# Performance work log

Measured on AMD Instinct MI355X. Metric: run time of the kernel, lower is better.

The kernel has to match this reference:

```python
import jax, jax.numpy as jnp
import numpy as np

EPS_CLAMP = 1e-6
TAU2 = 1.0


def _l2norm_rows(x):
    # F.normalize(x, p=2, dim=1) with eps=1e-12
    n = jnp.sqrt(jnp.sum(x * x, axis=1, keepdims=True))
    return x / jnp.maximum(n, 1e-12)


def _ws_v22(x_mean, x_std):
    m = _l2norm_rows(x_mean)                      # [N, F]
    c = _l2norm_rows(jnp.exp(x_std))              # [N, F]
    sq = jnp.sum(m * m, axis=1)                   # [N]
    # squared euclidean pairwise distance (cdist(...)**2)
    d2 = jnp.maximum(sq[:, None] + sq[None, :] - 2.0 * (m @ m.T), 0.0)
    csum = jnp.sum(c, axis=1)                     # [N]
    cs = jnp.sqrt(c)
    res = d2 + csum[:, None] + csum[None, :] - 2.0 * (cs @ cs.T)
    return jnp.exp(-res)                          # [N, N]


def _gcn_conv_dense(A, x, W, b):
    # PyG GCNConv with dense weighted adjacency A (A[i,j] = weight of edge i->j),
    # add_remaining_self_loops(fill=1), deg over target (column sums),
    # norm_ij = d_i^-1/2 * A_ij * d_j^-1/2, aggregate at target: out = A_norm^T @ (xW) + b
    diag = jnp.diagonal(A)
    A = A + jnp.diag(jnp.where(diag > 0, 0.0, 1.0))  # add self-loop weight 1 only where missing
    deg = jnp.sum(A, axis=0)                         # column sums (target degree)
    dis = jnp.where(deg > 0, deg ** -0.5, 0.0)
    An = dis[:, None] * A * dis[None, :]
    return An.T @ (x @ W) + b


def _encoder(A, x, W0, b0, W1, b1):
    h = jax.nn.relu(_gcn_conv_dense(A, x, W0, b0))
    return jax.nn.relu(_gcn_conv_dense(A, h, W1, b1))


def setup_inputs() -> dict:
    key = jax.random.key(0)
    ks = jax.random.split(key, 16)
    N, F, H = 4096, 512, 256
    s_in = 1.0 / np.sqrt(F)
    s_h = 1.0 / np.sqrt(2 * H)
    inp = {
        "x": jax.random.normal(ks[0], (N, F), dtype=jnp.float32),
        "new_edge": jax.random.uniform(ks[1], (N, N), dtype=jnp.float32),
        "beta": jax.random.uniform(ks[2], (1,), dtype=jnp.float32),
        "delta": jax.random.uniform(ks[3], (1,), dtype=jnp.float32),
        "eps": jax.random.uniform(ks[4], (N, N), dtype=jnp.float32),
        "Wm": jax.random.uniform(ks[5], (F, F), jnp.float32, -s_in, s_in),
        "bm": jax.random.uniform(ks[6], (F,), jnp.float32, -s_in, s_in),
        "Ws": jax.random.uniform(ks[7], (F, F), jnp.float32, -s_in, s_in),
        "bs": jax.random.uniform(ks[8], (F,), jnp.float32, -s_in, s_in),
        "mW0": jax.random.uniform(ks[9], (F, 2 * H), jnp.float32, -s_in, s_in) ,
        "mb0": jnp.zeros((2 * H,), jnp.float32),
        "mW1": jax.random.uniform(ks[10], (2 * H, H), jnp.float32, -s_h, s_h),
        "mb1": jnp.zeros((H,), jnp.float32),
        "sW0": jax.random.uniform(ks[11], (F, 2 * H), jnp.float32, -s_in, s_in),
        "sb0": jnp.zeros((2 * H,), jnp.float32),
        "sW1": jax.random.uniform(ks[12], (2 * H, H), jnp.float32, -s_h, s_h),
        "sb1": jnp.zeros((H,), jnp.float32),
    }
    return inp


def reference(x, new_edge, beta, delta, eps, Wm, bm, Ws, bs,
              mW0, mb0, mW1, mb1, sW0, sb0, sW1, sb1):
    b = beta[0]
    d = delta[0]
    x_mean = x @ Wm + bm
    x_std = x @ Ws + bs
    ws = _l2norm_rows(_ws_v22(x_mean, x_std))       # F.normalize(WS_v22(...)) row-wise
    term = (1.0 - b) * ws + b * new_edge
    term = jnp.clip(term, EPS_CLAMP, 1.0 - EPS_CLAMP)
    term = jnp.log(term / (1.0 - term))
    e = jnp.clip(eps, EPS_CLAMP, 1.0 - EPS_CLAMP)
    term = term + jnp.log(e / (1.0 - e))
    term = jax.nn.sigmoid(term / TAU2)
    term = jnp.where(term > d, term, 0.0)           # dense sparsified adjacency
    z_mean = _encoder(term, x_mean, mW0, mb0, mW1, mb1)
    z_std = _encoder(term, x_std, sW0, sb0, sW1, sb1)
    return z_mean, z_std
```

## Files before the change

### kernel.cpp

```cpp
#include <hip/hip_runtime.h>
#include <cstddef>

static constexpr int kN = 4096;
static constexpr int kF = 512;
static constexpr int kH = 256;
static constexpr float kClamp = 1e-6f;

using bf16x8 = __attribute__((ext_vector_type(8))) __bf16;
using f32x4 = __attribute__((ext_vector_type(4))) float;
using ushort8 = __attribute__((ext_vector_type(8))) unsigned short;
using ushort4v = __attribute__((ext_vector_type(4))) unsigned short;

static constexpr size_t PLANE_XF = (size_t)kN * kF;
static constexpr size_t PLANE_NN = (size_t)kN * kN;
static constexpr size_t PLANE_W = (size_t)512 * 512;
static constexpr size_t PLANE_W1 = (size_t)256 * 512;
static constexpr size_t PLANE_V0 = (size_t)1024 * kN;
static constexpr size_t PLANE_H = (size_t)kN * 1024;
static constexpr size_t PLANE_V1 = (size_t)512 * kN;

__device__ __forceinline__ unsigned short f2bf(float x) {
  unsigned int u = __float_as_uint(x);
  u += 0x7fffu + ((u >> 16) & 1u);
  return (unsigned short)(u >> 16);
}
__device__ __forceinline__ float bf2f(unsigned short h) {
  return __uint_as_float(((unsigned int)h) << 16);
}
__device__ __forceinline__ void split3(float x, unsigned short& h,
                                       unsigned short& m, unsigned short& l) {
  h = f2bf(x);
  const float r1 = x - bf2f(h);
  m = f2bf(r1);
  l = f2bf(r1 - bf2f(m));
}
__device__ __forceinline__ void split2(float x, unsigned short& h,
                                       unsigned short& m) {
  h = f2bf(x);
  m = f2bf(x - bf2f(h));
}
__device__ __forceinline__ void split2x4(const float4 v, ushort4v& h4,
                                         ushort4v& m4) {
  unsigned short h, m;
  split2(v.x, h, m); h4.x = h; m4.x = m;
  split2(v.y, h, m); h4.y = h; m4.y = m;
  split2(v.z, h, m); h4.z = h; m4.z = m;
  split2(v.w, h, m); h4.w = h; m4.w = m;
}

__device__ __forceinline__ bf16x8 ldfrag(const unsigned short* p) {
  ushort8 r = *(const ushort8*)p;
  return __builtin_bit_cast(bf16x8, r);
}
__device__ __forceinline__ f32x4 mfma16(bf16x8 a, bf16x8 b, f32x4 c) {
  return __builtin_amdgcn_mfma_f32_16x16x32_bf16(a, b, c, 0, 0, 0);
}
__device__ __forceinline__ f32x4 mfma_split6(const bf16x8* a3, const bf16x8* b3,
                                             f32x4 acc) {
  acc = mfma16(a3[2], b3[0], acc);
  acc = mfma16(a3[0], b3[2], acc);
  acc = mfma16(a3[1], b3[1], acc);
  acc = mfma16(a3[1], b3[0], acc);
  acc = mfma16(a3[0], b3[1], acc);
  acc = mfma16(a3[0], b3[0], acc);
  return acc;
}

__device__ __forceinline__ void tri_map(int b, int& bi, int& bj) {
  int x = (int)((sqrtf(8.0f * (float)b + 1.0f) - 1.0f) * 0.5f);
  while ((x + 1) * (x + 2) / 2 <= b) ++x;
  while (x * (x + 1) / 2 > b) --x;
  bi = x;
  bj = b - x * (x + 1) / 2;
}

__device__ __forceinline__ float block_reduce_sum(float v, float* sbuf) {
  const int tid = threadIdx.x;
  sbuf[tid] = v;
  __syncthreads();
#pragma unroll
  for (int s = 128; s > 0; s >>= 1) {
    if (tid < s) sbuf[tid] += sbuf[tid + s];
    __syncthreads();
  }
  const float r = sbuf[0];
  __syncthreads();
  return r;
}

__global__ __launch_bounds__(256) void prep_w(
    const float* s0, const float* s1, const float* s2, const float* s3,
    const float* s4, const float* s5, unsigned short* d0, unsigned short* d1,
    unsigned short* d2, unsigned short* d3, unsigned short* d4,
    unsigned short* d5) {
  const int seg = blockIdx.y;
  const float* src;
  unsigned short* dst;
  int N;
  bool tri;
  switch (seg) {
    case 0: src = s0; dst = d0; N = 512; tri = true; break;
    case 1: src = s1; dst = d1; N = 512; tri = true; break;
    case 2: src = s2; dst = d2; N = 512; tri = false; break;
    case 3: src = s3; dst = d3; N = 512; tri = false; break;
    case 4: src = s4; dst = d4; N = 256; tri = false; break;
    default: src = s5; dst = d5; N = 256; tri = false; break;
  }
  const int id = blockIdx.x * 256 + threadIdx.x;
  if (id >= 512 * N) return;
  const int k = id & 511;
  const int n = id >> 9;
  const float v = src[(size_t)k * N + n];
  const size_t base = (size_t)n * 512 + k;
  const size_t plane = (size_t)512 * N;
  if (tri) {
    unsigned short h, m, l;
    split3(v, h, m, l);
    dst[base] = h;
    dst[plane + base] = m;
    dst[2 * plane + base] = l;
  } else {
    unsigned short h, m;
    split2(v, h, m);
    dst[base] = h;
    dst[plane + base] = m;
  }
}

__global__ __launch_bounds__(256) void split_x(const float* __restrict__ x,
                                               unsigned short* __restrict__ x3) {
  const size_t id = (size_t)blockIdx.x * 256 + threadIdx.x;
  unsigned short h, m, l;
  split3(x[id], h, m, l);
  x3[id] = h;
  x3[PLANE_XF + id] = m;
  x3[2 * PLANE_XF + id] = l;
}

__global__ __launch_bounds__(256) void gemm_x(
    const unsigned short* __restrict__ A3, const unsigned short* __restrict__ B30,
    const unsigned short* __restrict__ B31, float* __restrict__ C0,
    float* __restrict__ C1, const float* __restrict__ bias0,
    const float* __restrict__ bias1) {
  constexpr int BM = 128, BN = 64, K = 512;
  __shared__ __align__(16) unsigned short Asl[3][BM][40];
  __shared__ __align__(16) unsigned short Bsl[3][BN][40];
  const int tid = threadIdx.x;
  const int lane = tid & 63;
  const int wave = tid >> 6;
  const int wm = wave >> 1, wn = wave & 1;
  const int m0 = blockIdx.y * BM;
  const int n0 = blockIdx.x * BN;
  const bool str1 = (n0 >= 512);
  const int nloc = str1 ? (n0 - 512) : n0;
  const unsigned short* Bb = str1 ? B31 : B30;
  const float* bias = str1 ? bias1 : bias0;
  float* C = str1 ? C1 : C0;
  const int rl = lane & 15;
  const int kq = (lane >> 4) * 8;
  const int q = lane >> 4;

  f32x4 acc[4][2];
#pragma unroll
  for (int i = 0; i < 4; ++i)
#pragma unroll
    for (int j = 0; j < 2; ++j) acc[i][j] = (f32x4){0.f, 0.f, 0.f, 0.f};

  for (int k0 = 0; k0 < K; k0 += 32) {
#pragma unroll
    for (int it = 0; it < 6; ++it) {
      const int c = tid + it * 256;
      const int plane = c / (BM * 4);
      const int rem = c % (BM * 4);
      const int row = rem >> 2;
      const int kc = (rem & 3) * 8;
      const ushort8 v = *(const ushort8*)(&A3[(size_t)plane * PLANE_XF +
                                              (size_t)(m0 + row) * K + k0 + kc]);
      *(ushort8*)(&Asl[plane][row][kc]) = v;
    }
#pragma unroll
    for (int it = 0; it < 3; ++it) {
      const int c = tid + it * 256;
      const int plane = c / (BN * 4);
      const int rem = c % (BN * 4);
      const int row = rem >> 2;
      const int kc = (rem & 3) * 8;
      const ushort8 v = *(const ushort8*)(&Bb[(size_t)plane * PLANE_W +
                                              (size_t)(nloc + row) * K + k0 + kc]);
      *(ushort8*)(&Bsl[plane][row][kc]) = v;
    }
    __syncthreads();
    bf16x8 af[4][3], bfr[2][3];
#pragma unroll
    for (int mt = 0; mt < 4; ++mt)
#pragma unroll
      for (int t = 0; t < 3; ++t)
        af[mt][t] = ldfrag(&Asl[t][wm * 64 + mt * 16 + rl][kq]);
#pragma unroll
    for (int nt = 0; nt < 2; ++nt)
#pragma unroll
      for (int t = 0; t < 3; ++t)
        bfr[nt][t] = ldfrag(&Bsl[t][wn * 32 + nt * 16 + rl][kq]);
#pragma unroll
    for (int mt = 0; mt < 4; ++mt)
#pragma unroll
      for (int nt = 0; nt < 2; ++nt)
        acc[mt][nt] = mfma_split6(af[mt], bfr[nt], acc[mt][nt]);
    __syncthreads();
  }
#pragma unroll
  for (int mt = 0; mt < 4; ++mt)
#pragma unroll
    for (int nt = 0; nt < 2; ++nt) {
      const int col = nloc + wn * 32 + nt * 16 + rl;
      const int row0 = m0 + wm * 64 + mt * 16 + q * 4;
      const float bv = bias[col];
#pragma unroll
      for (int r = 0; r < 4; ++r)
        C[(size_t)(row0 + r) * 512 + col] = acc[mt][nt][r] + bv;
    }
}

template <int BM, int BN>
__global__ __launch_bounds__(256) void gemm2ct(
    const unsigned short* __restrict__ A0, const unsigned short* __restrict__ A1,
    int lda, size_t planeA, const unsigned short* __restrict__ B0,
    const unsigned short* __restrict__ B1, int ldb, size_t planeB,
    unsigned short* __restrict__ Cs0, unsigned short* __restrict__ Cs1, int ldc,
    size_t planeC, int N1, int K, const float* __restrict__ rowScale) {
  __shared__ __align__(16) unsigned short Asl[2][BM][40];
  __shared__ __align__(16) unsigned short Bsl[2][BN][40];
  const int tid = threadIdx.x;
  const int lane = tid & 63;
  const int wave = tid >> 6;
  const int wm = wave >> 1, wn = wave & 1;
  const int m0 = blockIdx.y * BM;
  const int n0 = blockIdx.x * BN;
  const bool str1 = (n0 >= N1);
  const int nloc = str1 ? (n0 - N1) : n0;
  const unsigned short* Ab = str1 ? A1 : A0;
  const unsigned short* Bb = str1 ? B1 : B0;
  const int rl = lane & 15;
  const int kq = (lane >> 4) * 8;
  const int q = lane >> 4;
  constexpr int MT = BM / 32;
  constexpr int NT = BN / 32;

  f32x4 acc[MT][NT];
#pragma unroll
  for (int i = 0; i < MT; ++i)
#pragma unroll
    for (int j = 0; j < NT; ++j) acc[i][j] = (f32x4){0.f, 0.f, 0.f, 0.f};

  for (int k0 = 0; k0 < K; k0 += 32) {
    constexpr int AIT = (2 * BM * 4) / 256;
#pragma unroll
    for (int it = 0; it < AIT; ++it) {
      const int c = tid + it * 256;
      const int plane = c / (BM * 4);
      const int rem = c % (BM * 4);
      const int row = rem >> 2;
      const int kc = (rem & 3) * 8;
      const ushort8 v = *(const ushort8*)(&Ab[(size_t)plane * planeA +
                                              (size_t)(m0 + row) * lda + k0 + kc]);
      *(ushort8*)(&Asl[plane][row][kc]) = v;
    }
    constexpr int BIT = (2 * BN * 4) / 256;
#pragma unroll
    for (int it = 0; it < BIT; ++it) {
      const int c = tid + it * 256;
      const int plane = c / (BN * 4);
      const int rem = c % (BN * 4);
      const int row = rem >> 2;
      const int kc = (rem & 3) * 8;
      const ushort8 v = *(const ushort8*)(&Bb[(size_t)plane * planeB +
                                              (size_t)(nloc + row) * ldb + k0 + kc]);
      *(ushort8*)(&Bsl[plane][row][kc]) = v;
    }
    __syncthreads();
    bf16x8 af[MT][2];
#pragma unroll
    for (int mt = 0; mt < MT; ++mt)
#pragma unroll
      for (int t = 0; t < 2; ++t)
        af[mt][t] = ldfrag(&Asl[t][wm * (BM / 2) + mt * 16 + rl][kq]);
#pragma unroll
    for (int nt = 0; nt < NT; ++nt) {
      const bf16x8 b0 = ldfrag(&Bsl[0][wn * (BN / 2) + nt * 16 + rl][kq]);
      const bf16x8 b1 = ldfrag(&Bsl[1][wn * (BN / 2) + nt * 16 + rl][kq]);
#pragma unroll
      for (int mt = 0; mt < MT; ++mt) {
        acc[mt][nt] = mfma16(af[mt][1], b0, acc[mt][nt]);
        acc[mt][nt] = mfma16(af[mt][0], b1, acc[mt][nt]);
        acc[mt][nt] = mfma16(af[mt][0], b0, acc[mt][nt]);
      }
    }
    __syncthreads();
  }

#pragma unroll
  for (int mt = 0; mt < MT; ++mt) {
#pragma unroll
    for (int nt = 0; nt < NT; ++nt) {
      const int colL = nloc + wn * (BN / 2) + nt * 16 + rl;
      const int row0 = m0 + wm * (BM / 2) + mt * 16 + q * 4;
      float4 v4;
      float* vp = &v4.x;
#pragma unroll
      for (int r = 0; r < 4; ++r) {
        float v = acc[mt][nt][r];
        if (rowScale) v *= rowScale[row0 + r];
        vp[r] = v;
      }
      unsigned short* C = str1 ? Cs1 : Cs0;
      ushort4v h4, m4;
      split2x4(v4, h4, m4);
      const size_t base = (size_t)colL * ldc + row0;
      *(ushort4v*)(&C[base]) = h4;
      *(ushort4v*)(&C[planeC + base]) = m4;
    }
  }
}

template <int BM, int BN, int GX, int GYP, int GZ>
__global__ __launch_bounds__(256) void gemm2k(
    const unsigned short* __restrict__ A, int lda, size_t planeA,
    const unsigned short* __restrict__ B, int ldb, size_t planeB,
    float* __restrict__ Cp, int ldc, int Mtot, int Ksl) {
  __shared__ __align__(16) unsigned short Asl[2][BM][40];
  __shared__ __align__(16) unsigned short Bsl[2][BN][40];
  const int lin = blockIdx.x;
  const int xcd = lin & 7;
  const int s = lin >> 3;
  constexpr int per = GX * GYP;
  const int z = s / per;
  const int r = s - z * per;
  const int bx = r % GX;
  const int by = xcd * GYP + r / GX;
  const int m0 = by * BM;
  const int n0 = bx * BN;
  const int kOff = z * Ksl;

  const int tid = threadIdx.x;
  const int lane = tid & 63;
  const int wave = tid >> 6;
  const int wm = wave >> 1, wn = wave & 1;
  const int rl = lane & 15;
  const int kq = (lane >> 4) * 8;
  const int q = lane >> 4;
  constexpr int MT = BM / 32;
  constexpr int NT = BN / 32;

  f32x4 acc[MT][NT];
#pragma unroll
  for (int i = 0; i < MT; ++i)
#pragma unroll
    for (int j = 0; j < NT; ++j) acc[i][j] = (f32x4){0.f, 0.f, 0.f, 0.f};

  for (int k0 = 0; k0 < Ksl; k0 += 32) {
    constexpr int AIT = (2 * BM * 4) / 256;
#pragma unroll
    for (int it = 0; it < AIT; ++it) {
      const int c = tid + it * 256;
      const int plane = c / (BM * 4);
      const int rem = c % (BM * 4);
      const int row = rem >> 2;
      const int kc = (rem & 3) * 8;
      const ushort8 v = *(const ushort8*)(&A[(size_t)plane * planeA +
                                             (size_t)(m0 + row) * lda + kOff +
                                             k0 + kc]);
      *(ushort8*)(&Asl[plane][row][kc]) = v;
    }
    constexpr int BIT = (2 * BN * 4) / 256;
#pragma unroll
    for (int it = 0; it < BIT; ++it) {
      const int c = tid + it * 256;
      const int plane = c / (BN * 4);
      const int rem = c % (BN * 4);
      const int row = rem >> 2;
      const int kc = (rem & 3) * 8;
      const ushort8 v = *(const ushort8*)(&B[(size_t)plane * planeB +
                                             (size_t)(n0 + row) * ldb + kOff +
                                             k0 + kc]);
      *(ushort8*)(&Bsl[plane][row][kc]) = v;
    }
    __syncthreads();
    bf16x8 af[MT][2];
#pragma unroll
    for (int mt = 0; mt < MT; ++mt)
#pragma unroll
      for (int t = 0; t < 2; ++t)
        af[mt][t] = ldfrag(&Asl[t][wm * (BM / 2) + mt * 16 + rl][kq]);
#pragma unroll
    for (int nt = 0; nt < NT; ++nt) {
      const bf16x8 b0 = ldfrag(&Bsl[0][wn * (BN / 2) + nt * 16 + rl][kq]);
      const bf16x8 b1 = ldfrag(&Bsl[1][wn * (BN / 2) + nt * 16 + rl][kq]);
#pragma unroll
      for (int mt = 0; mt < MT; ++mt) {
        acc[mt][nt] = mfma16(af[mt][1], b0, acc[mt][nt]);
        acc[mt][nt] = mfma16(af[mt][0], b1, acc[mt][nt]);
        acc[mt][nt] = mfma16(af[mt][0], b0, acc[mt][nt]);
      }
    }
    __syncthreads();
  }

  const size_t zoff = (size_t)z * (size_t)Mtot * (size_t)ldc;
#pragma unroll
  for (int mt = 0; mt < MT; ++mt) {
#pragma unroll
    for (int nt = 0; nt < NT; ++nt) {
      const int colL = n0 + wn * (BN / 2) + nt * 16 + rl;
      const int row0 = m0 + wm * (BM / 2) + mt * 16 + q * 4;
#pragma unroll
      for (int r = 0; r < 4; ++r)
        Cp[zoff + (size_t)(row0 + r) * ldc + colL] = acc[mt][nt][r];
    }
  }
}

__global__ __launch_bounds__(256) void row_stats(
    const float* __restrict__ XMf, const float* __restrict__ XSf,
    unsigned short* __restrict__ M2, unsigned short* __restrict__ CS2,
    unsigned short* __restrict__ XM2, unsigned short* __restrict__ XS2,
    float* __restrict__ sq, float* __restrict__ csum) {
  __shared__ float sbuf[256];
  const int i = blockIdx.x;
  const int tid = threadIdx.x;
  const size_t base = (size_t)i * kF;
  const size_t i0 = base + tid, i1 = base + tid + 256;
  const float x0 = XMf[i0], x1 = XMf[i1];
  {
    unsigned short h, m;
    split2(x0, h, m);
    XM2[i0] = h; XM2[PLANE_XF + i0] = m;
    split2(x1, h, m);
    XM2[i1] = h; XM2[PLANE_XF + i1] = m;
  }
  const float nrm = block_reduce_sum(x0 * x0 + x1 * x1, sbuf);
  const float inv = 1.0f / fmaxf(sqrtf(nrm), 1e-12f);
  const float m0 = x0 * inv, m1 = x1 * inv;
  {
    unsigned short h, m;
    split2(m0, h, m);
    M2[i0] = h; M2[PLANE_XF + i0] = m;
    split2(m1, h, m);
    M2[i1] = h; M2[PLANE_XF + i1] = m;
  }
  const float s2 = block_reduce_sum(m0 * m0 + m1 * m1, sbuf);
  if (tid == 0) sq[i] = s2;

  const float y0 = XSf[i0], y1 = XSf[i1];
  {
    unsigned short h, m;
    split2(y0, h, m);
    XS2[i0] = h; XS2[PLANE_XF + i0] = m;
    split2(y1, h, m);
    XS2[i1] = h; XS2[PLANE_XF + i1] = m;
  }
  const float e0 = expf(y0), e1 = expf(y1);
  const float nrm2 = block_reduce_sum(e0 * e0 + e1 * e1, sbuf);
  const float inv2 = 1.0f / fmaxf(sqrtf(nrm2), 1e-12f);
  const float c0 = e0 * inv2, c1 = e1 * inv2;
  const float sc = block_reduce_sum(c0 + c1, sbuf);
  if (tid == 0) csum[i] = sc;
  {
    unsigned short h, m;
    split2(sqrtf(c0), h, m);
    CS2[i0] = h; CS2[PLANE_XF + i0] = m;
    split2(sqrtf(c1), h, m);
    CS2[i1] = h; CS2[PLANE_XF + i1] = m;
  }
}

__global__ __launch_bounds__(256) void ws_mfma2(
    const unsigned short* __restrict__ M2, const unsigned short* __restrict__ CS2,
    const float* __restrict__ sq, const float* __restrict__ csum,
    float* __restrict__ WSR) {
  __shared__ __align__(16) unsigned short S[4][2][64][40];
  int bi, bj;
  tri_map(blockIdx.x, bi, bj);
  const int i0 = bi * 64, j0 = bj * 64;
  const int tid = threadIdx.x;
  const int lane = tid & 63;
  const int wave = tid >> 6;
  const int wm = wave >> 1, wn = wave & 1;
  const int rl = lane & 15;
  const int kq = (lane >> 4) * 8;
  const int q = lane >> 4;

  f32x4 aM[2][2], aC[2][2];
#pragma unroll
  for (int i = 0; i < 2; ++i)
#pragma unroll
    for (int j = 0; j < 2; ++j) {
      aM[i][j] = (f32x4){0.f, 0.f, 0.f, 0.f};
      aC[i][j] = (f32x4){0.f, 0.f, 0.f, 0.f};
    }

  for (int k0 = 0; k0 < kF; k0 += 32) {
#pragma unroll
    for (int it = 0; it < 8; ++it) {
      const int c = tid + it * 256;
      const int op = c >> 9;
      const int rem = c & 511;
      const int plane = rem >> 8;
      const int r2 = rem & 255;
      const int row = r2 >> 2;
      const int kc = (r2 & 3) * 8;
      const unsigned short* mat = (op & 1) ? CS2 : M2;
      const int rowoff = (op < 2) ? i0 : j0;
      const ushort8 v = *(const ushort8*)(&mat[(size_t)plane * PLANE_XF +
                                               (size_t)(rowoff + row) * kF + k0 +
                                               kc]);
      *(ushort8*)(&S[op][plane][row][kc]) = v;
    }
    __syncthreads();
    bf16x8 am[2][2], ac[2][2], bm[2][2], bc[2][2];
#pragma unroll
    for (int mt = 0; mt < 2; ++mt)
#pragma unroll
      for (int t = 0; t < 2; ++t) {
        am[mt][t] = ldfrag(&S[0][t][wm * 32 + mt * 16 + rl][kq]);
        ac[mt][t] = ldfrag(&S[1][t][wm * 32 + mt * 16 + rl][kq]);
      }
#pragma unroll
    for (int nt = 0; nt < 2; ++nt)
#pragma unroll
      for (int t = 0; t < 2; ++t) {
        bm[nt][t] = ldfrag(&S[2][t][wn * 32 + nt * 16 + rl][kq]);
        bc[nt][t] = ldfrag(&S[3][t][wn * 32 + nt * 16 + rl][kq]);
      }
#pragma unroll
    for (int mt = 0; mt < 2; ++mt)
#pragma unroll
      for (int nt = 0; nt < 2; ++nt) {
        aM[mt][nt] = mfma16(am[mt][1], bm[nt][0], aM[mt][nt]);
        aM[mt][nt] = mfma16(am[mt][0], bm[nt][1], aM[mt][nt]);
        aM[mt][nt] = mfma16(am[mt][0], bm[nt][0], aM[mt][nt]);
        aC[mt][nt] = mfma16(ac[mt][1], bc[nt][0], aC[mt][nt]);
        aC[mt][nt] = mfma16(ac[mt][0], bc[nt][1], aC[mt][nt]);
        aC[mt][nt] = mfma16(ac[mt][0], bc[nt][0], aC[mt][nt]);
      }
    __syncthreads();
  }

#pragma unroll
  for (int mt = 0; mt < 2; ++mt) {
#pragma unroll
    for (int nt = 0; nt < 2; ++nt) {
      const int j = j0 + wn * 32 + nt * 16 + rl;
      const int ib = i0 + wm * 32 + mt * 16 + q * 4;
      const float sqj = sq[j], csj = csum[j];
      float4 vv;
      float* vp = &vv.x;
#pragma unroll
      for (int r = 0; r < 4; ++r) {
        const int i = ib + r;
        const float d2 = fmaxf(sq[i] + sqj - 2.0f * aM[mt][nt][r], 0.0f);
        const float res = d2 + csum[i] + csj - 2.0f * aC[mt][nt][r];
        const float v = expf(-res);
        vp[r] = v;
        WSR[(size_t)i * kN + j] = v;
      }
      if (bi != bj) *(float4*)(&WSR[(size_t)j * kN + ib]) = vv;
    }
  }
}

__global__ __launch_bounds__(256) void row_invnorm_kernel(
    const float* __restrict__ WSR, float* __restrict__ invn) {
  __shared__ float sbuf[256];
  const int i = blockIdx.x;
  const int tid = threadIdx.x;
  const float4* rp = (const float4*)(WSR + (size_t)i * kN);
  float s = 0.0f;
#pragma unroll
  for (int q = 0; q < (kN / 4) / 256; ++q) {
    const float4 v = rp[tid + q * 256];
    s += v.x * v.x + v.y * v.y + v.z * v.z + v.w * v.w;
  }
  s = block_reduce_sum(s, sbuf);
  if (tid == 0) invn[i] = 1.0f / fmaxf(sqrtf(s), 1e-12f);
}

__device__ __forceinline__ float adj_val(float w, float inv, float nev, float ev,
                                         float b, float d, bool diag) {
  float t = (1.0f - b) * (w * inv) + b * nev;
  t = fminf(fmaxf(t, kClamp), 1.0f - kClamp);
  float L = logf(t / (1.0f - t));
  const float e = fminf(fmaxf(ev, kClamp), 1.0f - kClamp);
  L += logf(e / (1.0f - e));
  const float s = 1.0f / (1.0f + expf(-L));
  float v = (s > d) ? s : 0.0f;
  if (diag) v = (v > 0.0f) ? v : 1.0f;
  return v;
}

__global__ __launch_bounds__(256) void adj_transpose(
    const float* __restrict__ WSR, const float* __restrict__ invn,
    const float* __restrict__ ne, const float* __restrict__ epsm,
    const float* __restrict__ beta_p, const float* __restrict__ delta_p,
    unsigned short* __restrict__ Adj2, float* __restrict__ degp) {
  __shared__ float T0[64][65];
  __shared__ float T1[64][65];
  const float b = beta_p[0];
  const float d = delta_p[0];
  int bi, bj;
  tri_map(blockIdx.x, bi, bj);
  const int i0 = bi * 64, j0 = bj * 64;
  const int tid = threadIdx.x;
  const int rlq = tid >> 4;
  const int cq = (tid & 15) * 4;
#pragma unroll
  for (int p = 0; p < 4; ++p) {
    const int ii = p * 16 + rlq;
    {
      const size_t off = (size_t)(i0 + ii) * kN + j0 + cq;
      const float4 w4 = *(const float4*)(&WSR[off]);
      const float4 n4 = *(const float4*)(&ne[off]);
      const float4 e4 = *(const float4*)(&epsm[off]);
      const float inv = invn[i0 + ii];
      const float wv[4] = {w4.x, w4.y, w4.z, w4.w};
      const float nv[4] = {n4.x, n4.y, n4.z, n4.w};
      const float ev[4] = {e4.x, e4.y, e4.z, e4.w};
#pragma unroll
      for (int u = 0; u < 4; ++u)
        T0[ii][cq + u] =
            adj_val(wv[u], inv, nv[u], ev[u], b, d, (i0 + ii) == (j0 + cq + u));
    }
    if (bi != bj) {
      const size_t off = (size_t)(j0 + ii) * kN + i0 + cq;
      const float4 w4 = *(const float4*)(&WSR[off]);
      const float4 n4 = *(const float4*)(&ne[off]);
      const float4 e4 = *(const float4*)(&epsm[off]);
      const float inv = invn[j0 + ii];
      const float wv[4] = {w4.x, w4.y, w4.z, w4.w};
      const float nv[4] = {n4.x, n4.y, n4.z, n4.w};
      const float ev[4] = {e4.x, e4.y, e4.z, e4.w};
#pragma unroll
      for (int u = 0; u < 4; ++u)
        T1[ii][cq + u] = adj_val(wv[u], inv, nv[u], ev[u], b, d, false);
    }
  }
  __syncthreads();
#pragma unroll
  for (int p = 0; p < 4; ++p) {
    const int jj = p * 16 + rlq;
    {
      const float4 v4 = make_float4(T0[cq + 0][jj], T0[cq + 1][jj],
                                    T0[cq + 2][jj], T0[cq + 3][jj]);
      ushort4v h4, m4;
      split2x4(v4, h4, m4);
      const size_t base = (size_t)(j0 + jj) * kN + i0 + cq;
      *(ushort4v*)(&Adj2[base]) = h4;
      *(ushort4v*)(&Adj2[PLANE_NN + base]) = m4;
    }
    if (bi != bj) {
      const float4 v4 = make_float4(T1[cq + 0][jj], T1[cq + 1][jj],
                                    T1[cq + 2][jj], T1[cq + 3][jj]);
      ushort4v h4, m4;
      split2x4(v4, h4, m4);
      const size_t base = (size_t)(i0 + jj) * kN + j0 + cq;
      *(ushort4v*)(&Adj2[base]) = h4;
      *(ushort4v*)(&Adj2[PLANE_NN + base]) = m4;
    }
  }
  if (tid < 64) {
    float s = 0.0f;
#pragma unroll 8
    for (int ii = 0; ii < 64; ++ii) s += T0[ii][tid];
    degp[(size_t)bi * kN + j0 + tid] = s;
    if (bi != bj) {
      float s1 = 0.0f;
#pragma unroll 8
      for (int ii = 0; ii < 64; ++ii) s1 += T1[ii][tid];
      degp[(size_t)bj * kN + i0 + tid] = s1;
    }
  }
}

__global__ __launch_bounds__(256) void deg_dis_kernel(
    const float* __restrict__ degp, float* __restrict__ dis) {
  const int j = blockIdx.x * 256 + threadIdx.x;
  float s = 0.0f;
#pragma unroll
  for (int c = 0; c < 64; ++c) s += degp[(size_t)c * kN + j];
  dis[j] = (s > 0.0f) ? (1.0f / sqrtf(s)) : 0.0f;
}

__global__ __launch_bounds__(256) void combine_h(
    const float* __restrict__ hp, const float* __restrict__ dis,
    const float* __restrict__ b0, const float* __restrict__ b1,
    unsigned short* __restrict__ h2) {
  const size_t qd = (size_t)blockIdx.x * 256 + threadIdx.x;
  const int m = (int)(qd >> 8);
  const int c0 = (int)(qd & 255) * 4;
  const size_t off = (size_t)m * 1024 + c0;
  const float4 s0 = *(const float4*)(&hp[off]);
  const float4 s1 = *(const float4*)(&hp[PLANE_H + off]);
  const float4 s2 = *(const float4*)(&hp[2 * PLANE_H + off]);
  const float4 s3 = *(const float4*)(&hp[3 * PLANE_H + off]);
  const float4 bv = (c0 < 512) ? *(const float4*)(&b0[c0])
                               : *(const float4*)(&b1[c0 - 512]);
  const float ds = dis[m];
  float4 v4;
  v4.x = fmaxf(ds * (s0.x + s1.x + s2.x + s3.x) + bv.x, 0.f);
  v4.y = fmaxf(ds * (s0.y + s1.y + s2.y + s3.y) + bv.y, 0.f);
  v4.z = fmaxf(ds * (s0.z + s1.z + s2.z + s3.z) + bv.z, 0.f);
  v4.w = fmaxf(ds * (s0.w + s1.w + s2.w + s3.w) + bv.w, 0.f);
  ushort4v h4, m4;
  split2x4(v4, h4, m4);
  *(ushort4v*)(&h2[off]) = h4;
  *(ushort4v*)(&h2[PLANE_H + off]) = m4;
}

__global__ __launch_bounds__(256) void combine_z(
    const float* __restrict__ zp, const float* __restrict__ dis,
    const float* __restrict__ b0, const float* __restrict__ b1,
    float* __restrict__ out) {
  const size_t qd = (size_t)blockIdx.x * 256 + threadIdx.x;
  const int m = (int)(qd >> 7);
  const int c0 = (int)(qd & 127) * 4;
  const size_t off = (size_t)m * 512 + c0;
  constexpr size_t PZ = (size_t)kN * 512;
  const float4 s0 = *(const float4*)(&zp[off]);
  const float4 s1 = *(const float4*)(&zp[PZ + off]);
  const float4 s2 = *(const float4*)(&zp[2 * PZ + off]);
  const float4 s3 = *(const float4*)(&zp[3 * PZ + off]);
  const float4 bv = (c0 < 256) ? *(const float4*)(&b0[c0])
                               : *(const float4*)(&b1[c0 - 256]);
  const float ds = dis[m];
  float4 v4;
  v4.x = fmaxf(ds * (s0.x + s1.x + s2.x + s3.x) + bv.x, 0.f);
  v4.y = fmaxf(ds * (s0.y + s1.y + s2.y + s3.y) + bv.y, 0.f);
  v4.z = fmaxf(ds * (s0.z + s1.z + s2.z + s3.z) + bv.z, 0.f);
  v4.w = fmaxf(ds * (s0.w + s1.w + s2.w + s3.w) + bv.w, 0.f);
  float* dst = (c0 < 256) ? &out[(size_t)m * 256 + c0]
                          : &out[(size_t)kN * 256 + (size_t)m * 256 + (c0 - 256)];
  *(float4*)dst = v4;
}

extern "C" void kernel_launch(void* const* d_in, const int* in_sizes, int n_in,
                              void* d_out, int out_size, void* d_ws,
                              size_t ws_size, hipStream_t stream) {
  const float* x = (const float*)d_in[0];
  const float* ne = (const float*)d_in[1];
  const float* beta = (const float*)d_in[2];
  const float* delta = (const float*)d_in[3];
  const float* epsm = (const float*)d_in[4];
  const float* Wm = (const float*)d_in[5];
  const float* bm = (const float*)d_in[6];
  const float* Ws = (const float*)d_in[7];
  const float* bs = (const float*)d_in[8];
  const float* mW0 = (const float*)d_in[9];
  const float* mb0 = (const float*)d_in[10];
  const float* mW1 = (const float*)d_in[11];
  const float* mb1 = (const float*)d_in[12];
  const float* sW0 = (const float*)d_in[13];
  const float* sb0 = (const float*)d_in[14];
  const float* sW1 = (const float*)d_in[15];
  const float* sb1 = (const float*)d_in[16];
  float* out = (float*)d_out;

  char* p = (char*)d_ws;
  float* WSR = (float*)p;                     p += PLANE_NN * 4;
  unsigned short* Adj2 = (unsigned short*)p;  p += 2 * PLANE_NN * 2;
  unsigned short* x3 = (unsigned short*)p;    p += 3 * PLANE_XF * 2;
  float* XMf = (float*)p;                     p += PLANE_XF * 4;
  float* XSf = (float*)p;                     p += PLANE_XF * 4;
  unsigned short* XM2 = (unsigned short*)p;   p += 2 * PLANE_XF * 2;
  unsigned short* XS2 = (unsigned short*)p;   p += 2 * PLANE_XF * 2;
  unsigned short* M2 = (unsigned short*)p;    p += 2 * PLANE_XF * 2;
  unsigned short* CS2 = (unsigned short*)p;   p += 2 * PLANE_XF * 2;
  unsigned short* Wm3 = (unsigned short*)p;   p += 3 * PLANE_W * 2;
  unsigned short* Ws3 = (unsigned short*)p;   p += 3 * PLANE_W * 2;
  unsigned short* mW0t2 = (unsigned short*)p; p += 2 * PLANE_W * 2;
  unsigned short* sW0t2 = (unsigned short*)p; p += 2 * PLANE_W * 2;
  unsigned short* mW1t2 = (unsigned short*)p; p += 2 * PLANE_W1 * 2;
  unsigned short* sW1t2 = (unsigned short*)p; p += 2 * PLANE_W1 * 2;
  float* degp = (float*)p;                    p += (size_t)64 * kN * 4;
  float* sq = (float*)p;                      p += kN * 4;
  float* csum = (float*)p;                    p += kN * 4;
  float* invn = (float*)p;                    p += kN * 4;
  float* dis = (float*)p;                     p += kN * 4;

  float* hp = WSR;
  float* zp = WSR;
  unsigned short* V1t2 = x3;
  unsigned short* h2 = XM2;
  unsigned short* V0t2 = M2;

  const dim3 blk(256);
  const int nTri = (kN / 64) * (kN / 64 + 1) / 2;

  prep_w<<<dim3(1024, 6), blk, 0, stream>>>(Wm, Ws, mW0, sW0, mW1, sW1, Wm3,
                                            Ws3, mW0t2, sW0t2, mW1t2, sW1t2);
  split_x<<<(kN * kF) / 256, blk, 0, stream>>>(x, x3);

  gemm_x<<<dim3(16, 32), blk, 0, stream>>>(x3, Wm3, Ws3, XMf, XSf, bm, bs);

  row_stats<<<kN, blk, 0, stream>>>(XMf, XSf, M2, CS2, XM2, XS2, sq, csum);

  ws_mfma2<<<nTri, blk, 0, stream>>>(M2, CS2, sq, csum, WSR);

  row_invnorm_kernel<<<kN, blk, 0, stream>>>(WSR, invn);

  adj_transpose<<<nTri, blk, 0, stream>>>(WSR, invn, ne, epsm, beta, delta,
                                          Adj2, degp);
  deg_dis_kernel<<<kN / 256, blk, 0, stream>>>(degp, dis);

  gemm2ct<128, 64><<<dim3(16, 32), blk, 0, stream>>>(
      XM2, XS2, kF, PLANE_XF, mW0t2, sW0t2, kF, PLANE_W, V0t2,
      V0t2 + (size_t)512 * kN, kN, PLANE_V0, 512, kF, dis);

  gemm2k<128, 128, 8, 4, 4><<<1024, blk, 0, stream>>>(
      Adj2, kN, PLANE_NN, V0t2, kN, PLANE_V0, hp, 1024, kN, kN / 4);
  combine_h<<<(int)(PLANE_H / 4 / 256), blk, 0, stream>>>(hp, dis, mb0, sb0, h2);

  gemm2ct<64, 64><<<dim3(8, 64), blk, 0, stream>>>(
      h2, h2 + 512, 1024, PLANE_H, mW1t2, sW1t2, kF, PLANE_W1, V1t2,
      V1t2 + (size_t)256 * kN, kN, PLANE_V1, 256, kF, dis);

  gemm2k<128, 128, 4, 4, 4><<<512, blk, 0, stream>>>(
      Adj2, kN, PLANE_NN, V1t2, kN, PLANE_V1, zp, 512, kN, kN / 4);
  combine_z<<<(int)((size_t)kN * 512 / 4 / 256), blk, 0, stream>>>(zp, dis, mb1,
                                                                   sb1, out);
}
```

Measured before the change: 634.1 us.

## Rewrite adjacency GEMM as 256x256 tiled, 8-wave, double-buffered direct-to-LDS pipeline

Replaces the 128x128 split-K adjacency GEMM with a 512-thread kernel that computes 256x256 tiles. It stages A and B straight into LDS with global_load_lds and double-buffers them, interleaving the refills with four MFMA phases per k-step that use setprio and barriers. The second GEMM raises split-K from 4 to 8 so the grid stays at 256 blocks, and combine_z now sums 8 partial planes. This aims to raise data reuse per tile and overlap memory with MFMA, at the cost of more partial-sum traffic in the second stage, tight vmcnt bookkeeping and heavy register pressure.

```diff
diff --git a/kernel.cpp b/kernel.cpp
--- a/kernel.cpp
+++ b/kernel.cpp
@@ -64,6 +64,13 @@
   acc = mfma16(a3[0], b3[1], acc);
   acc = mfma16(a3[0], b3[0], acc);
   return acc;
+}
+
+__device__ __forceinline__ void gload16(const unsigned short* g,
+                                        unsigned short* l) {
+  __builtin_amdgcn_global_load_lds(
+      (const __attribute__((address_space(1))) void*)g,
+      (__attribute__((address_space(3))) void*)l, 16, 0, 0);
 }
 
 __device__ __forceinline__ void tri_map(int b, int& bi, int& bj) {
@@ -322,13 +329,32 @@
   }
 }
 
-template <int BM, int BN, int GX, int GYP, int GZ>
-__global__ __launch_bounds__(256) void gemm2k(
+#define GK8_READ_A(P, AF)                                                   \
+  {                                                                         \
+    _Pragma("unroll") for (int e = 0; e < 2; ++e)                           \
+        _Pragma("unroll") for (int pl = 0; pl < 2; ++pl)                    \
+            AF[e][pl] = ldfrag(&Abuf[cur][P][pl][wm][e * 16 + rl][kq]);     \
+  }
+#define GK8_MFMA(P, AF)                                                     \
+  {                                                                         \
+    _Pragma("unroll") for (int e = 0; e < 2; ++e)                           \
+        _Pragma("unroll") for (int nt = 0; nt < 4; ++nt) {                  \
+      acc[2 * (P) + e][nt] =                                                \
+          mfma16(AF[e][1], bfr[nt][0], acc[2 * (P) + e][nt]);               \
+      acc[2 * (P) + e][nt] =                                                \
+          mfma16(AF[e][0], bfr[nt][1], acc[2 * (P) + e][nt]);               \
+      acc[2 * (P) + e][nt] =                                                \
+          mfma16(AF[e][0], bfr[nt][0], acc[2 * (P) + e][nt]);               \
+    }                                                                       \
+  }
+
+template <int GX, int GYP, int GZ>
+__global__ __launch_bounds__(512, 2) void gemm2k8(
     const unsigned short* __restrict__ A, int lda, size_t planeA,
     const unsigned short* __restrict__ B, int ldb, size_t planeB,
     float* __restrict__ Cp, int ldc, int Mtot, int Ksl) {
-  __shared__ __align__(16) unsigned short Asl[2][BM][40];
-  __shared__ __align__(16) unsigned short Bsl[2][BN][40];
+  __shared__ __align__(16) unsigned short Abuf[2][4][2][2][32][32];
+  __shared__ __align__(16) unsigned short Bbuf[2][2][256][32];
   const int lin = blockIdx.x;
   const int xcd = lin & 7;
   const int s = lin >> 3;
@@ -337,84 +363,123 @@
   const int r = s - z * per;
   const int bx = r % GX;
   const int by = xcd * GYP + r / GX;
-  const int m0 = by * BM;
-  const int n0 = bx * BN;
+  const int m0 = by * 256;
+  const int n0 = bx * 256;
   const int kOff = z * Ksl;
+  const int ntk = Ksl >> 5;
 
   const int tid = threadIdx.x;
   const int lane = tid & 63;
   const int wave = tid >> 6;
-  const int wm = wave >> 1, wn = wave & 1;
+  const int wm = wave >> 2;
+  const int wn = wave & 3;
   const int rl = lane & 15;
   const int kq = (lane >> 4) * 8;
   const int q = lane >> 4;
-  constexpr int MT = BM / 32;
-  constexpr int NT = BN / 32;
-
-  f32x4 acc[MT][NT];
-#pragma unroll
-  for (int i = 0; i < MT; ++i)
-#pragma unroll
-    for (int j = 0; j < NT; ++j) acc[i][j] = (f32x4){0.f, 0.f, 0.f, 0.f};
-
-  for (int k0 = 0; k0 < Ksl; k0 += 32) {
-    constexpr int AIT = (2 * BM * 4) / 256;
-#pragma unroll
-    for (int it = 0; it < AIT; ++it) {
-      const int c = tid + it * 256;
-      const int plane = c / (BM * 4);
-      const int rem = c % (BM * 4);
-      const int row = rem >> 2;
-      const int kc = (rem & 3) * 8;
-      const ushort8 v = *(const ushort8*)(&A[(size_t)plane * planeA +
-                                             (size_t)(m0 + row) * lda + kOff +
-                                             k0 + kc]);
-      *(ushort8*)(&Asl[plane][row][kc]) = v;
-    }
-    constexpr int BIT = (2 * BN * 4) / 256;
-#pragma unroll
-    for (int it = 0; it < BIT; ++it) {
-      const int c = tid + it * 256;
-      const int plane = c / (BN * 4);
-      const int rem = c % (BN * 4);
-      const int row = rem >> 2;
-      const int kc = (rem & 3) * 8;
-      const ushort8 v = *(const ushort8*)(&B[(size_t)plane * planeB +
-                                             (size_t)(n0 + row) * ldb + kOff +
-                                             k0 + kc]);
-      *(ushort8*)(&Bsl[plane][row][kc]) = v;
-    }
-    __syncthreads();
-    bf16x8 af[MT][2];
-#pragma unroll
-    for (int mt = 0; mt < MT; ++mt)
-#pragma unroll
-      for (int t = 0; t < 2; ++t)
-        af[mt][t] = ldfrag(&Asl[t][wm * (BM / 2) + mt * 16 + rl][kq]);
-#pragma unroll
-    for (int nt = 0; nt < NT; ++nt) {
-      const bf16x8 b0 = ldfrag(&Bsl[0][wn * (BN / 2) + nt * 16 + rl][kq]);
-      const bf16x8 b1 = ldfrag(&Bsl[1][wn * (BN / 2) + nt * 16 + rl][kq]);
-#pragma unroll
-      for (int mt = 0; mt < MT; ++mt) {
-        acc[mt][nt] = mfma16(af[mt][1], b0, acc[mt][nt]);
-        acc[mt][nt] = mfma16(af[mt][0], b1, acc[mt][nt]);
-        acc[mt][nt] = mfma16(af[mt][0], b0, acc[mt][nt]);
-      }
-    }
-    __syncthreads();
+
+  const int stRow = tid >> 2;
+  const int stSlot = (tid & 3) * 8;
+  const int aPl = tid >> 8;
+  const int aHalf = (tid >> 7) & 1;
+  const int aR = (tid >> 2) & 31;
+
+  auto stageB = [&](int bi, int kt, int c) {
+    const unsigned short* src = B + (size_t)(c >> 1) * planeB +
+                                (size_t)(n0 + (c & 1) * 128 + stRow) * ldb +
+                                kOff + kt * 32 + stSlot;
+    unsigned short* dst = &Bbuf[bi][0][0][0] + c * 4096 + wave * 512;
+    gload16(src, dst);
+  };
+  auto stageA = [&](int bi, int kt, int p) {
+    const unsigned short* src =
+        A + (size_t)aPl * planeA +
+        (size_t)(m0 + aHalf * 128 + p * 32 + aR) * lda + kOff + kt * 32 +
+        stSlot;
+    unsigned short* dst = &Abuf[bi][0][0][0][0][0] + p * 4096 + wave * 512;
+    gload16(src, dst);
+  };
+
+  f32x4 acc[8][4];
+#pragma unroll
+  for (int i = 0; i < 8; ++i)
+#pragma unroll
+    for (int j = 0; j < 4; ++j) acc[i][j] = (f32x4){0.f, 0.f, 0.f, 0.f};
+
+#pragma unroll
+  for (int c = 0; c < 4; ++c) stageB(0, 0, c);
+#pragma unroll
+  for (int p = 0; p < 4; ++p) stageA(0, 0, p);
+#pragma unroll
+  for (int c = 0; c < 4; ++c) stageB(1, 1, c);
+#pragma unroll
+  for (int p = 0; p < 4; ++p) stageA(1, 1, p);
+  asm volatile("s_waitcnt vmcnt(8)" ::: "memory");
+  __builtin_amdgcn_s_barrier();
+
+  for (int t = 0; t < ntk; ++t) {
+    const int cur = t & 1;
+    const bool refill = (t + 2 < ntk);
+    if (t >= 1 && t + 1 < ntk) stageA(cur ^ 1, t + 1, 3);
+    bf16x8 bfr[4][2];
+#pragma unroll
+    for (int nt = 0; nt < 4; ++nt)
+#pragma unroll
+      for (int pl = 0; pl < 2; ++pl)
+        bfr[nt][pl] = ldfrag(&Bbuf[cur][pl][wn * 64 + nt * 16 + rl][kq]);
+    bf16x8 af0[2][2];
+    GK8_READ_A(0, af0);
+    __builtin_amdgcn_s_barrier();
+    __builtin_amdgcn_s_setprio(1);
+    GK8_MFMA(0, af0);
+    __builtin_amdgcn_s_setprio(0);
+    __builtin_amdgcn_s_barrier();
+    if (refill) {
+      stageB(cur, t + 2, 0);
+      stageB(cur, t + 2, 1);
+      stageB(cur, t + 2, 2);
+      stageB(cur, t + 2, 3);
+      stageA(cur, t + 2, 0);
+    }
+    bf16x8 af1[2][2];
+    GK8_READ_A(1, af1);
+    __builtin_amdgcn_s_barrier();
+    __builtin_amdgcn_s_setprio(1);
+    GK8_MFMA(1, af1);
+    __builtin_amdgcn_s_setprio(0);
+    __builtin_amdgcn_s_barrier();
+    if (refill) stageA(cur, t + 2, 1);
+    bf16x8 af2[2][2];
+    GK8_READ_A(2, af2);
+    __builtin_amdgcn_s_barrier();
+    __builtin_amdgcn_s_setprio(1);
+    GK8_MFMA(2, af2);
+    __builtin_amdgcn_s_setprio(0);
+    __builtin_amdgcn_s_barrier();
+    if (refill) stageA(cur, t + 2, 2);
+    bf16x8 af3[2][2];
+    GK8_READ_A(3, af3);
+    __builtin_amdgcn_s_barrier();
+    __builtin_amdgcn_s_setprio(1);
+    GK8_MFMA(3, af3);
+    __builtin_amdgcn_s_setprio(0);
+    if (refill) {
+      asm volatile("s_waitcnt vmcnt(7)" ::: "memory");
+    } else {
+      asm volatile("s_waitcnt vmcnt(0)" ::: "memory");
+    }
+    __builtin_amdgcn_s_barrier();
   }
 
   const size_t zoff = (size_t)z * (size_t)Mtot * (size_t)ldc;
 #pragma unroll
-  for (int mt = 0; mt < MT; ++mt) {
-#pragma unroll
-    for (int nt = 0; nt < NT; ++nt) {
-      const int colL = n0 + wn * (BN / 2) + nt * 16 + rl;
-      const int row0 = m0 + wm * (BM / 2) + mt * 16 + q * 4;
-#pragma unroll
-      for (int r = 0; r < 4; ++r)
-        Cp[zoff + (size_t)(row0 + r) * ldc + colL] = acc[mt][nt][r];
+  for (int mt = 0; mt < 8; ++mt) {
+#pragma unroll
+    for (int nt = 0; nt < 4; ++nt) {
+      const int col = n0 + wn * 64 + nt * 16 + rl;
+      const int row0 = m0 + wm * 128 + mt * 16 + q * 4;
+#pragma unroll
+      for (int r2 = 0; r2 < 4; ++r2)
+        Cp[zoff + (size_t)(row0 + r2) * ldc + col] = acc[mt][nt][r2];
     }
   }
 }
@@ -724,18 +789,23 @@
   const int c0 = (int)(qd & 127) * 4;
   const size_t off = (size_t)m * 512 + c0;
   constexpr size_t PZ = (size_t)kN * 512;
-  const float4 s0 = *(const float4*)(&zp[off]);
-  const float4 s1 = *(const float4*)(&zp[PZ + off]);
-  const float4 s2 = *(const float4*)(&zp[2 * PZ + off]);
-  const float4 s3 = *(const float4*)(&zp[3 * PZ + off]);
+  float4 a = *(const float4*)(&zp[off]);
+#pragma unroll
+  for (int i = 1; i < 8; ++i) {
+    const float4 si = *(const float4*)(&zp[(size_t)i * PZ + off]);
+    a.x += si.x;
+    a.y += si.y;
+    a.z += si.z;
+    a.w += si.w;
+  }
   const float4 bv = (c0 < 256) ? *(const float4*)(&b0[c0])
                                : *(const float4*)(&b1[c0 - 256]);
   const float ds = dis[m];
   float4 v4;
-  v4.x = fmaxf(ds * (s0.x + s1.x + s2.x + s3.x) + bv.x, 0.f);
-  v4.y = fmaxf(ds * (s0.y + s1.y + s2.y + s3.y) + bv.y, 0.f);
-  v4.z = fmaxf(ds * (s0.z + s1.z + s2.z + s3.z) + bv.z, 0.f);
-  v4.w = fmaxf(ds * (s0.w + s1.w + s2.w + s3.w) + bv.w, 0.f);
+  v4.x = fmaxf(ds * a.x + bv.x, 0.f);
+  v4.y = fmaxf(ds * a.y + bv.y, 0.f);
+  v4.z = fmaxf(ds * a.z + bv.z, 0.f);
+  v4.w = fmaxf(ds * a.w + bv.w, 0.f);
   float* dst = (c0 < 256) ? &out[(size_t)m * 256 + c0]
                           : &out[(size_t)kN * 256 + (size_t)m * 256 + (c0 - 256)];
   *(float4*)dst = v4;
@@ -814,7 +884,7 @@
       XM2, XS2, kF, PLANE_XF, mW0t2, sW0t2, kF, PLANE_W, V0t2,
       V0t2 + (size_t)512 * kN, kN, PLANE_V0, 512, kF, dis);
 
-  gemm2k<128, 128, 8, 4, 4><<<1024, blk, 0, stream>>>(
+  gemm2k8<4, 2, 4><<<256, dim3(512), 0, stream>>>(
       Adj2, kN, PLANE_NN, V0t2, kN, PLANE_V0, hp, 1024, kN, kN / 4);
   combine_h<<<(int)(PLANE_H / 4 / 256), blk, 0, stream>>>(hp, dis, mb0, sb0, h2);
 
@@ -822,8 +892,8 @@
       h2, h2 + 512, 1024, PLANE_H, mW1t2, sW1t2, kF, PLANE_W1, V1t2,
       V1t2 + (size_t)256 * kN, kN, PLANE_V1, 256, kF, dis);
 
-  gemm2k<128, 128, 4, 4, 4><<<512, blk, 0, stream>>>(
-      Adj2, kN, PLANE_NN, V1t2, kN, PLANE_V1, zp, 512, kN, kN / 4);
+  gemm2k8<2, 2, 8><<<256, dim3(512), 0, stream>>>(
+      Adj2, kN, PLANE_NN, V1t2, kN, PLANE_V1, zp, 512, kN, kN / 8);
   combine_z<<<(int)((size_t)kN * 512 / 4 / 256), blk, 0, stream>>>(zp, dis, mb1,
                                                                    sb1, out);
 }
```

Measured after the change: 664.5 us. 4.8% more time.
